# Kernel optimization log

Hardware: AMD Instinct MI355X
Metric: run time of the kernel (lower is better)

Reference implementation:

```python
import jax, jax.numpy as jnp
import numpy as np

H = 64
VOCAB = 64
SLOTS = 4
N_PASSES = 3
EPS = 1e-5


def _ln(x, g, b):
    m = jnp.mean(x, axis=-1, keepdims=True)
    v = jnp.mean((x - m) ** 2, axis=-1, keepdims=True)
    return (x - m) * jax.lax.rsqrt(v + EPS) * g + b


def setup_inputs() -> dict:
    key = jax.random.key(0)
    ks = iter(jax.random.split(key, 32))
    B, L = 128, 4096
    f = lambda shape, scale=0.05: jax.random.normal(next(ks), shape, dtype=jnp.float32) * scale
    inp = {
        "seq": jax.random.randint(next(ks), (B, L), 0, VOCAB),
        # Encoder
        "embed": f((VOCAB, H), 1.0),
        "ff1_w": f((H, 2 * H)), "ff1_b": jnp.zeros((2 * H,), jnp.float32),
        "ff2_w": f((2 * H, H)), "ff2_b": jnp.zeros((H,), jnp.float32),
        "enc_g": jnp.ones((H,), jnp.float32), "enc_b": jnp.zeros((H,), jnp.float32),
        # ForwardGate
        "g1_w": f((H, H // 2)), "g1_b": jnp.zeros((H // 2,), jnp.float32),
        "g2_w": f((H // 2, 1)), "g2_b": jnp.zeros((1,), jnp.float32),
        # Re-encoding layers (stacked over passes)
        "rq_w": f((N_PASSES, H, H)), "rq_b": jnp.zeros((N_PASSES, H), jnp.float32),
        "rk_w": f((N_PASSES, H, H)), "rk_b": jnp.zeros((N_PASSES, H), jnp.float32),
        "rv_w": f((N_PASSES, H, H)), "rv_b": jnp.zeros((N_PASSES, H), jnp.float32),
        "rn_g": jnp.ones((N_PASSES, H), jnp.float32), "rn_b": jnp.zeros((N_PASSES, H), jnp.float32),
        # ReadHead
        "rd_q_w": f((H, H)), "rd_q_b": jnp.zeros((H,), jnp.float32),
        "out_w": f((H, VOCAB)), "out_b": jnp.zeros((VOCAB,), jnp.float32),
    }
    return inp


def reference(seq, embed, ff1_w, ff1_b, ff2_w, ff2_b, enc_g, enc_b,
              g1_w, g1_b, g2_w, g2_b,
              rq_w, rq_b, rk_w, rk_b, rv_w, rv_b, rn_g, rn_b,
              rd_q_w, rd_q_b, out_w, out_b):
    scale = 1.0 / np.sqrt(H)
    # Encoder: embed + FFN residual + LayerNorm
    h = embed[seq]                                            # (B,L,H)
    ff = jax.nn.relu(h @ ff1_w + ff1_b) @ ff2_w + ff2_b
    hidden = _ln(h + ff, enc_g, enc_b)                        # (B,L,H)
    # Gate scores -> top-k slot selection
    scores = jax.nn.sigmoid(jax.nn.relu(hidden @ g1_w + g1_b) @ g2_w + g2_b)[..., 0]  # (B,L)
    _, idx = jax.lax.top_k(scores, SLOTS)                     # (B,k)
    slots = jnp.take_along_axis(hidden, idx[:, :, None], axis=1)  # (B,k,H)
    # Iterative cross-attention re-encoding
    for p in range(N_PASSES):
        Sq = slots @ rq_w[p] + rq_b[p]                        # (B,k,H)
        Sk = hidden @ rk_w[p] + rk_b[p]                       # (B,L,H)
        Sv = hidden @ rv_w[p] + rv_b[p]
        attn = jax.nn.softmax(jnp.einsum("bkh,blh->bkl", Sq, Sk) * scale, axis=-1)
        slots = _ln(slots + jnp.einsum("bkl,blh->bkh", attn, Sv), rn_g[p], rn_b[p])
    # Read head: attend last-token query over slots
    q = hidden[:, -1, :] @ rd_q_w + rd_q_b                    # (B,H)
    attn = jax.nn.softmax(jnp.einsum("bkh,bh->bk", slots, q) * scale, axis=-1)
    read = jnp.einsum("bk,bkh->bh", attn, slots)
    return read @ out_w + out_b                               # (B,VOCAB)
```

## Files before the change

### kernel.cpp

```cpp
#include <hip/hip_runtime.h>
#include <math.h>

#define H 64
#define VOCAB 64
#define LSEQ 4096
#define NSLOTS 4
#define NP 3
#define EPS 1e-5f
#define NBUILD 96

typedef unsigned long long ull;

__device__ __forceinline__ float wsum(float x) {
    #pragma unroll
    for (int m = 1; m < 64; m <<= 1) x += __shfl_xor(x, m);
    return x;
}
__device__ __forceinline__ float wmax(float x) {
    #pragma unroll
    for (int m = 1; m < 64; m <<= 1) x = fmaxf(x, __shfl_xor(x, m));
    return x;
}


__global__ __launch_bounds__(256) void build_and_hist(
    const int*   __restrict__ seq,
    const float* __restrict__ embed,
    const float* __restrict__ ff1_w, const float* __restrict__ ff1_b,
    const float* __restrict__ ff2_w, const float* __restrict__ ff2_b,
    const float* __restrict__ enc_g, const float* __restrict__ enc_b,
    const float* __restrict__ g1_w,  const float* __restrict__ g1_b,
    const float* __restrict__ g2_w,  const float* __restrict__ g2_b,
    const float* __restrict__ rq_w,  const float* __restrict__ rq_b,
    const float* __restrict__ rk_w,  const float* __restrict__ rk_b,
    const float* __restrict__ rv_w,  const float* __restrict__ rv_b,
    const float* __restrict__ rd_q_w, const float* __restrict__ rd_q_b,
    const float* __restrict__ out_w,
    float* __restrict__ enc_t, float* __restrict__ score_t,
    float* __restrict__ c_t, float* __restrict__ q_t,
    float* __restrict__ MT, float* __restrict__ SvT, float* __restrict__ owT,
    float* __restrict__ cnts_ws, int* __restrict__ lasts_ws)
{
    __shared__ float bld[4][320];
    __shared__ int   whist[4][64];

    const int bid = blockIdx.x, tid = threadIdx.x;
    const int wid = tid >> 6, lane = tid & 63;

    if (bid < NBUILD) {
        const int t   = bid * 4 + wid;
        const int seg = t >> 6, v = t & 63;
        float* h_s   = bld[wid];
        float* a1p   = bld[wid] + 64;
        float* hid_s = bld[wid] + 192;
        float* sk_s  = bld[wid] + 256;

        h_s[lane] = embed[v * H + lane];
        __builtin_amdgcn_wave_barrier();

        float pA[4] = {0, 0, 0, 0}, pB[4] = {0, 0, 0, 0};
        #pragma unroll
        for (int c4 = 0; c4 < 4; c4++)
            #pragma unroll
            for (int d = 0; d < 16; d++) {
                int dd = c4 * 16 + d;
                float hv = h_s[dd];
                pA[c4] += hv * ff1_w[dd * 128 + lane];
                pB[c4] += hv * ff1_w[dd * 128 + lane + 64];
            }
        a1p[lane]      = fmaxf(ff1_b[lane]      + ((pA[0] + pA[1]) + (pA[2] + pA[3])), 0.f);
        a1p[lane + 64] = fmaxf(ff1_b[lane + 64] + ((pB[0] + pB[1]) + (pB[2] + pB[3])), 0.f);
        __builtin_amdgcn_wave_barrier();

        float pO[4] = {0, 0, 0, 0};
        #pragma unroll
        for (int c4 = 0; c4 < 4; c4++)
            #pragma unroll
            for (int j = 0; j < 32; j++) {
                int jj = c4 * 32 + j;
                pO[c4] += a1p[jj] * ff2_w[jj * H + lane];
            }
        float o = ff2_b[lane] + ((pO[0] + pO[1]) + (pO[2] + pO[3]));

        float x = h_s[lane] + o;
        float s1 = x, s2 = x * x;
        #pragma unroll
        for (int m = 1; m < 64; m <<= 1) { s1 += __shfl_xor(s1, m); s2 += __shfl_xor(s2, m); }
        float mu  = s1 * (1.f / 64.f);
        float var = s2 * (1.f / 64.f) - mu * mu;
        float hid = (x - mu) * rsqrtf(var + EPS) * enc_g[lane] + enc_b[lane];
        hid_s[lane] = hid;
        __builtin_amdgcn_wave_barrier();

        if (seg == 0) {
            enc_t[v * H + lane] = hid;
            float p = 0.f;
            if (lane < 32) {
                float a[2] = {0, 0};
                #pragma unroll
                for (int c2 = 0; c2 < 2; c2++)
                    #pragma unroll
                    for (int d = 0; d < 32; d++) {
                        int dd = c2 * 32 + d;
                        a[c2] += hid_s[dd] * g1_w[dd * 32 + lane];
                    }
                p = fmaxf(g1_b[lane] + a[0] + a[1], 0.f) * g2_w[lane];
            }
            p = wsum(p);
            if (lane == 0) score_t[v] = 1.f / (1.f + expf(-(p + g2_b[0])));
            float qa[4] = {0, 0, 0, 0};
            #pragma unroll
            for (int c4 = 0; c4 < 4; c4++)
                #pragma unroll
                for (int d = 0; d < 16; d++) {
                    int dd = c4 * 16 + d;
                    qa[c4] += hid_s[dd] * rd_q_w[dd * H + lane];
                }
            q_t[v * H + lane] = rd_q_b[lane] + ((qa[0] + qa[1]) + (qa[2] + qa[3]));
        }
        if (seg < 3) {
            const int p = seg;
            float ka[4] = {0, 0, 0, 0};
            #pragma unroll
            for (int c4 = 0; c4 < 4; c4++)
                #pragma unroll
                for (int d = 0; d < 16; d++) {
                    int dd = c4 * 16 + d;
                    ka[c4] += hid_s[dd] * rk_w[(p * H + dd) * H + lane];
                }
            float skv = rk_b[p * H + lane] + ((ka[0] + ka[1]) + (ka[2] + ka[3]));
            sk_s[lane] = skv;
            float cpart = wsum(rq_b[p * H + lane] * skv);
            if (lane == 0) c_t[p * 64 + v] = cpart;
            __builtin_amdgcn_wave_barrier();
            const float4* rw4 = (const float4*)(rq_w + (size_t)(p * 64 + lane) * 64);
            const float4* sk4 = (const float4*)sk_s;
            float ma[4] = {0, 0, 0, 0};
            #pragma unroll
            for (int i = 0; i < 16; i++) {
                float4 w4 = rw4[i];
                float4 s4v = sk4[i];
                ma[0] += w4.x * s4v.x; ma[1] += w4.y * s4v.y;
                ma[2] += w4.z * s4v.z; ma[3] += w4.w * s4v.w;
            }
            MT[p * 4096 + v * 64 + lane] = ((ma[0] + ma[1]) + (ma[2] + ma[3]));
        } else {
            const int p = seg - 3;
            float va[4] = {0, 0, 0, 0};
            #pragma unroll
            for (int c4 = 0; c4 < 4; c4++)
                #pragma unroll
                for (int d = 0; d < 16; d++) {
                    int dd = c4 * 16 + d;
                    va[c4] += hid_s[dd] * rv_w[(p * H + dd) * H + lane];
                }
            float svv = rv_b[p * H + lane] + ((va[0] + va[1]) + (va[2] + va[3]));
            SvT[p * 4096 + lane * 64 + v] = svv;
            if (seg == 3) owT[v * 64 + lane] = out_w[lane * 64 + v];
        }
        return;
    }

    const int b = bid - NBUILD;
    const int4* s4 = (const int4*)(seq + (size_t)b * LSEQ);
    int4 t0 = s4[tid];
    int4 t1 = s4[tid + 256];
    int4 t2 = s4[tid + 512];
    int4 t3 = s4[tid + 768];
    whist[wid][lane] = 0;
    __builtin_amdgcn_wave_barrier();
    {
        int* hw = whist[wid];
        atomicAdd(&hw[t0.x], 1); atomicAdd(&hw[t0.y], 1);
        atomicAdd(&hw[t0.z], 1); atomicAdd(&hw[t0.w], 1);
        atomicAdd(&hw[t1.x], 1); atomicAdd(&hw[t1.y], 1);
        atomicAdd(&hw[t1.z], 1); atomicAdd(&hw[t1.w], 1);
        atomicAdd(&hw[t2.x], 1); atomicAdd(&hw[t2.y], 1);
        atomicAdd(&hw[t2.z], 1); atomicAdd(&hw[t2.w], 1);
        atomicAdd(&hw[t3.x], 1); atomicAdd(&hw[t3.y], 1);
        atomicAdd(&hw[t3.z], 1); atomicAdd(&hw[t3.w], 1);
    }
    __syncthreads();
    if (tid < 64)
        cnts_ws[b * 64 + tid] =
            (float)(whist[0][tid] + whist[1][tid] + whist[2][tid] + whist[3][tid]);
    if (tid == 255) lasts_ws[b] = t3.w;
}

#define PASS(P, MC, MN, CCV, RGV, RBV, LOADNEXT)                               \
{                                                                              \
    float4 vcur[16];                                                           \
    { const float4* b4 = (const float4*)(SvT + (P) * 4096 + lane * 64);        \
      _Pragma("unroll") for (int i = 0; i < 16; i++) vcur[i] = b4[i]; }        \
    if (LOADNEXT) {                                                            \
      const float4* b4 = (const float4*)(MT + ((P) + 1) * 4096 + lane * 64);   \
      _Pragma("unroll") for (int i = 0; i < 16; i++) MN[i] = b4[i]; }          \
    sls[wid][lane] = s;                                                        \
    const float4* sp = (const float4*)sls[wid];                                \
    float a0 = 0, a1x = 0, a2 = 0, a3 = 0;                                     \
    _Pragma("unroll") for (int i = 0; i < 16; i++) {                           \
        float4 s4v = sp[i];                                                    \
        a0 += s4v.x * MC[i].x; a1x += s4v.y * MC[i].y;                         \
        a2 += s4v.z * MC[i].z; a3 += s4v.w * MC[i].w; }                        \
    float lg = (CCV + ((a0 + a1x) + (a2 + a3))) * 0.125f;                      \
    float w  = cntf * __expf(lg);                                              \
    wls[wid][lane] = w;                                                        \
    float denom = wsum(w);                                                     \
    const float4* wp = (const float4*)wls[wid];                                \
    float b0 = 0, b1 = 0, b2 = 0, b3 = 0;                                      \
    _Pragma("unroll") for (int i = 0; i < 16; i++) {                           \
        float4 w4 = wp[i];                                                     \
        b0 += w4.x * vcur[i].x; b1 += w4.y * vcur[i].y;                        \
        b2 += w4.z * vcur[i].z; b3 += w4.w * vcur[i].w; }                      \
    float y = s * denom + ((b0 + b1) + (b2 + b3));                             \
    float s1 = y, s2v = y * y;                                                 \
    _Pragma("unroll") for (int m = 1; m < 64; m <<= 1) {                       \
        s1 += __shfl_xor(s1, m); s2v += __shfl_xor(s2v, m); }                  \
    float muy  = s1 * (1.f / 64.f);                                            \
    float vary = s2v * (1.f / 64.f) - muy * muy;                               \
    s = (y - muy) * rsqrtf(vary + EPS * denom * denom) * RGV + RBV;            \
}

__global__ __launch_bounds__(256) void run_batches(
    const float* __restrict__ score_t, const float* __restrict__ enc_t,
    const float* __restrict__ c_t, const float* __restrict__ q_t,
    const float* __restrict__ MT, const float* __restrict__ SvT,
    const float* __restrict__ owT,
    const float* __restrict__ rn_g, const float* __restrict__ rn_b,
    const float* __restrict__ out_b,
    const float* __restrict__ cnts_ws, const int* __restrict__ lasts_ws,
    float* __restrict__ out)
{
    __shared__ float sls[4][64], wls[4][64], slN[4][64];
    __shared__ float l4[4];
    __shared__ float rbuf[64];

    const int bid = blockIdx.x, tid = threadIdx.x;
    const int wid = tid >> 6, lane = tid & 63;

    const float cntf = cnts_ws[bid * 64 + lane];
    float sc  = score_t[lane];
    float cc0 = c_t[lane],  cc1 = c_t[64 + lane],  cc2 = c_t[128 + lane];
    float rg0 = rn_g[lane], rg1 = rn_g[64 + lane], rg2 = rn_g[128 + lane];
    float rb0 = rn_b[lane], rb1 = rn_b[64 + lane], rb2 = rn_b[128 + lane];
    float ob  = out_b[lane];

    float4 mA[16], mB[16], vA[16];
    {
        const float4* p4 = (const float4*)(MT + lane * 64);
        #pragma unroll
        for (int i = 0; i < 16; i++) mA[i] = p4[i];
        const float4* q4 = (const float4*)(SvT + lane * 64);
        #pragma unroll
        for (int i = 0; i < 16; i++) vA[i] = q4[i];
    }

    float mxs  = wmax(sc);
    ull   bm   = __ballot(sc == mxs);
    int   t_star = __ffsll(bm) - 1;
    int   nmax   = __popcll(bm);
    float cnt_ts = __shfl(cntf, t_star);
    const bool spec = (nmax == 1) && (cnt_ts >= 4.f);

    if (spec) {
        if (wid != 0) return;
        float s = enc_t[t_star * 64 + lane];

        {
            sls[0][lane] = s;
            const float4* sp = (const float4*)sls[0];
            float a0 = 0, a1x = 0, a2 = 0, a3 = 0;
            #pragma unroll
            for (int i = 0; i < 16; i++) {
                float4 s4v = sp[i];
                a0 += s4v.x * mA[i].x; a1x += s4v.y * mA[i].y;
                a2 += s4v.z * mA[i].z; a3 += s4v.w * mA[i].w;
            }
            float lg0 = (cc0 + ((a0 + a1x) + (a2 + a3))) * 0.125f;

            const float4* b4 = (const float4*)(MT + 4096 + lane * 64);
            #pragma unroll
            for (int i = 0; i < 16; i++) mB[i] = b4[i];

            float w = cntf * __expf(lg0);
            wls[0][lane] = w;
            float denom = wsum(w);
            const float4* wp = (const float4*)wls[0];
            float b0 = 0, b1 = 0, b2 = 0, b3 = 0;
            #pragma unroll
            for (int i = 0; i < 16; i++) {
                float4 w4 = wp[i];
                b0 += w4.x * vA[i].x; b1 += w4.y * vA[i].y;
                b2 += w4.z * vA[i].z; b3 += w4.w * vA[i].w;
            }
            float y = s * denom + ((b0 + b1) + (b2 + b3));
            float s1 = y, s2v = y * y;
            #pragma unroll
            for (int m = 1; m < 64; m <<= 1) { s1 += __shfl_xor(s1, m); s2v += __shfl_xor(s2v, m); }
            float muy  = s1 * (1.f / 64.f);
            float vary = s2v * (1.f / 64.f) - muy * muy;
            s = (y - muy) * rsqrtf(vary + EPS * denom * denom) * rg0 + rb0;
        }
        PASS(1, mB, mA, cc1, rg1, rb1, 1)
        PASS(2, mA, mB, cc2, rg2, rb2, 0)

        float4 ow[16];
        {
            const float4* b4 = (const float4*)(owT + lane * 64);
            #pragma unroll
            for (int i = 0; i < 16; i++) ow[i] = b4[i];
        }
        rbuf[lane] = s;
        __builtin_amdgcn_wave_barrier();
        const float4* rp = (const float4*)rbuf;
        float o0 = ob, o1 = 0.f, o2 = 0.f, o3 = 0.f;
        #pragma unroll
        for (int i = 0; i < 16; i++) {
            float4 rv = rp[i];
            o0 += rv.x * ow[i].x; o1 += rv.y * ow[i].y;
            o2 += rv.z * ow[i].z; o3 += rv.w * ow[i].w;
        }
        out[(size_t)bid * VOCAB + lane] = ((o0 + o1) + (o2 + o3));
        return;
    }

    const int cnt = (int)cntf;
    const int last = lasts_ws[bid];
    float q = q_t[last * 64 + lane];

    int my_tok = 0;
    {
        float key = cnt > 0 ? sc : -1.f;
        int filled = 0;
        bool have = false;
        #pragma unroll 1
        for (int r = 0; r < NSLOTS && filled < NSLOTS; r++) {
            float m2 = wmax(key);
            ull win = __ballot(key == m2);
            int tk = __ffsll(win) - 1;
            int c  = __shfl(cnt, tk);
            if (!have && (unsigned)(wid - filled) < (unsigned)c) { my_tok = tk; have = true; }
            filled += c;
            if (lane == tk) key = -1.f;
        }
    }

    float s = enc_t[my_tok * 64 + lane];

    PASS(0, mA, mB, cc0, rg0, rb0, 1)
    PASS(1, mB, mA, cc1, rg1, rb1, 1)
    PASS(2, mA, mB, cc2, rg2, rb2, 0)

    float lk = wsum(s * q) * 0.125f;
    if (lane == 0) l4[wid] = lk;
    slN[wid][lane] = s;

    float4 ow[16];
    if (wid == 0) {
        const float4* b4 = (const float4*)(owT + lane * 64);
        #pragma unroll
        for (int i = 0; i < 16; i++) ow[i] = b4[i];
    }
    __syncthreads();

    if (wid == 0) {
        float e0 = __expf(l4[0]), e1 = __expf(l4[1]);
        float e2 = __expf(l4[2]), e3 = __expf(l4[3]);
        float dn = e0 + e1 + e2 + e3;
        float r = (e0 * slN[0][lane] + e1 * slN[1][lane]
                 + e2 * slN[2][lane] + e3 * slN[3][lane]) / dn;
        rbuf[lane] = r;
        __builtin_amdgcn_wave_barrier();
        const float4* rp = (const float4*)rbuf;
        float o0 = ob, o1 = 0.f, o2 = 0.f, o3 = 0.f;
        #pragma unroll
        for (int i = 0; i < 16; i++) {
            float4 rv = rp[i];
            o0 += rv.x * ow[i].x; o1 += rv.y * ow[i].y;
            o2 += rv.z * ow[i].z; o3 += rv.w * ow[i].w;
        }
        out[(size_t)bid * VOCAB + lane] = ((o0 + o1) + (o2 + o3));
    }
}

extern "C" void kernel_launch(void* const* d_in, const int* in_sizes, int n_in,
                              void* d_out, int out_size, void* d_ws, size_t ws_size,
                              hipStream_t stream) {
    const int*   seq    = (const int*)  d_in[0];
    const float* embed  = (const float*)d_in[1];
    const float* ff1_w  = (const float*)d_in[2];
    const float* ff1_b  = (const float*)d_in[3];
    const float* ff2_w  = (const float*)d_in[4];
    const float* ff2_b  = (const float*)d_in[5];
    const float* enc_g  = (const float*)d_in[6];
    const float* enc_b  = (const float*)d_in[7];
    const float* g1_w   = (const float*)d_in[8];
    const float* g1_b   = (const float*)d_in[9];
    const float* g2_w   = (const float*)d_in[10];
    const float* g2_b   = (const float*)d_in[11];
    const float* rq_w   = (const float*)d_in[12];
    const float* rq_b   = (const float*)d_in[13];
    const float* rk_w   = (const float*)d_in[14];
    const float* rk_b   = (const float*)d_in[15];
    const float* rv_w   = (const float*)d_in[16];
    const float* rv_b   = (const float*)d_in[17];
    const float* rn_g   = (const float*)d_in[18];
    const float* rn_b   = (const float*)d_in[19];
    const float* rd_q_w = (const float*)d_in[20];
    const float* rd_q_b = (const float*)d_in[21];
    const float* out_w  = (const float*)d_in[22];
    const float* out_b  = (const float*)d_in[23];
    float* out = (float*)d_out;

    const int B = in_sizes[0] / LSEQ;

    float* ws      = (float*)d_ws;
    float* enc_t   = ws;
    float* score_t = ws + 4096;
    float* c_t     = ws + 4160;
    float* q_t     = ws + 4352;
    float* MT      = ws + 8448;
    float* SvT     = ws + 20736;
    float* owT     = ws + 33024;
    float* cnts_ws = ws + 37120;
    int*   lasts_ws = (int*)(ws + 37120 + (size_t)B * 64);

    build_and_hist<<<NBUILD + B, 256, 0, stream>>>(
        seq, embed, ff1_w, ff1_b, ff2_w, ff2_b, enc_g, enc_b,
        g1_w, g1_b, g2_w, g2_b,
        rq_w, rq_b, rk_w, rk_b, rv_w, rv_b,
        rd_q_w, rd_q_b, out_w,
        enc_t, score_t, c_t, q_t, MT, SvT, owT, cnts_ws, lasts_ws);

    run_batches<<<B, 256, 0, stream>>>(
        score_t, enc_t, c_t, q_t, MT, SvT, owT,
        rn_g, rn_b, out_b, cnts_ws, lasts_ws, out);
}
```

Before: 24.75 us.

## Fuse build and batch kernels into one launch with global flag spin-wait

Merges the table-building/histogram kernel and the per-batch attention kernel into a single launch. Build blocks signal completion through an atomic counter, and batch blocks compute their histogram and then spin until all build blocks are done before reading the shared tables. This removes a kernel launch boundary and the global round-trip for counts and last tokens. In exchange it adds a memset launch and relies on all build blocks being co-resident or scheduled ahead, which risks deadlock or spin overhead.

After: 46.17 us. 86.5% more time.

```diff
diff --git a/kernel.cpp b/kernel.cpp
--- a/kernel.cpp
+++ b/kernel.cpp
@@ -8,6 +8,7 @@
 #define NP 3
 #define EPS 1e-5f
 #define NBUILD 96
+#define FLAG_OFF (1u << 20)
 
 typedef unsigned long long ull;
 
@@ -22,170 +23,6 @@
     return x;
 }
 
-
-__global__ __launch_bounds__(256) void build_and_hist(
-    const int*   __restrict__ seq,
-    const float* __restrict__ embed,
-    const float* __restrict__ ff1_w, const float* __restrict__ ff1_b,
-    const float* __restrict__ ff2_w, const float* __restrict__ ff2_b,
-    const float* __restrict__ enc_g, const float* __restrict__ enc_b,
-    const float* __restrict__ g1_w,  const float* __restrict__ g1_b,
-    const float* __restrict__ g2_w,  const float* __restrict__ g2_b,
-    const float* __restrict__ rq_w,  const float* __restrict__ rq_b,
-    const float* __restrict__ rk_w,  const float* __restrict__ rk_b,
-    const float* __restrict__ rv_w,  const float* __restrict__ rv_b,
-    const float* __restrict__ rd_q_w, const float* __restrict__ rd_q_b,
-    const float* __restrict__ out_w,
-    float* __restrict__ enc_t, float* __restrict__ score_t,
-    float* __restrict__ c_t, float* __restrict__ q_t,
-    float* __restrict__ MT, float* __restrict__ SvT, float* __restrict__ owT,
-    float* __restrict__ cnts_ws, int* __restrict__ lasts_ws)
-{
-    __shared__ float bld[4][320];
-    __shared__ int   whist[4][64];
-
-    const int bid = blockIdx.x, tid = threadIdx.x;
-    const int wid = tid >> 6, lane = tid & 63;
-
-    if (bid < NBUILD) {
-        const int t   = bid * 4 + wid;
-        const int seg = t >> 6, v = t & 63;
-        float* h_s   = bld[wid];
-        float* a1p   = bld[wid] + 64;
-        float* hid_s = bld[wid] + 192;
-        float* sk_s  = bld[wid] + 256;
-
-        h_s[lane] = embed[v * H + lane];
-        __builtin_amdgcn_wave_barrier();
-
-        float pA[4] = {0, 0, 0, 0}, pB[4] = {0, 0, 0, 0};
-        #pragma unroll
-        for (int c4 = 0; c4 < 4; c4++)
-            #pragma unroll
-            for (int d = 0; d < 16; d++) {
-                int dd = c4 * 16 + d;
-                float hv = h_s[dd];
-                pA[c4] += hv * ff1_w[dd * 128 + lane];
-                pB[c4] += hv * ff1_w[dd * 128 + lane + 64];
-            }
-        a1p[lane]      = fmaxf(ff1_b[lane]      + ((pA[0] + pA[1]) + (pA[2] + pA[3])), 0.f);
-        a1p[lane + 64] = fmaxf(ff1_b[lane + 64] + ((pB[0] + pB[1]) + (pB[2] + pB[3])), 0.f);
-        __builtin_amdgcn_wave_barrier();
-
-        float pO[4] = {0, 0, 0, 0};
-        #pragma unroll
-        for (int c4 = 0; c4 < 4; c4++)
-            #pragma unroll
-            for (int j = 0; j < 32; j++) {
-                int jj = c4 * 32 + j;
-                pO[c4] += a1p[jj] * ff2_w[jj * H + lane];
-            }
-        float o = ff2_b[lane] + ((pO[0] + pO[1]) + (pO[2] + pO[3]));
-
-        float x = h_s[lane] + o;
-        float s1 = x, s2 = x * x;
-        #pragma unroll
-        for (int m = 1; m < 64; m <<= 1) { s1 += __shfl_xor(s1, m); s2 += __shfl_xor(s2, m); }
-        float mu  = s1 * (1.f / 64.f);
-        float var = s2 * (1.f / 64.f) - mu * mu;
-        float hid = (x - mu) * rsqrtf(var + EPS) * enc_g[lane] + enc_b[lane];
-        hid_s[lane] = hid;
-        __builtin_amdgcn_wave_barrier();
-
-        if (seg == 0) {
-            enc_t[v * H + lane] = hid;
-            float p = 0.f;
-            if (lane < 32) {
-                float a[2] = {0, 0};
-                #pragma unroll
-                for (int c2 = 0; c2 < 2; c2++)
-                    #pragma unroll
-                    for (int d = 0; d < 32; d++) {
-                        int dd = c2 * 32 + d;
-                        a[c2] += hid_s[dd] * g1_w[dd * 32 + lane];
-                    }
-                p = fmaxf(g1_b[lane] + a[0] + a[1], 0.f) * g2_w[lane];
-            }
-            p = wsum(p);
-            if (lane == 0) score_t[v] = 1.f / (1.f + expf(-(p + g2_b[0])));
-            float qa[4] = {0, 0, 0, 0};
-            #pragma unroll
-            for (int c4 = 0; c4 < 4; c4++)
-                #pragma unroll
-                for (int d = 0; d < 16; d++) {
-                    int dd = c4 * 16 + d;
-                    qa[c4] += hid_s[dd] * rd_q_w[dd * H + lane];
-                }
-            q_t[v * H + lane] = rd_q_b[lane] + ((qa[0] + qa[1]) + (qa[2] + qa[3]));
-        }
-        if (seg < 3) {
-            const int p = seg;
-            float ka[4] = {0, 0, 0, 0};
-            #pragma unroll
-            for (int c4 = 0; c4 < 4; c4++)
-                #pragma unroll
-                for (int d = 0; d < 16; d++) {
-                    int dd = c4 * 16 + d;
-                    ka[c4] += hid_s[dd] * rk_w[(p * H + dd) * H + lane];
-                }
-            float skv = rk_b[p * H + lane] + ((ka[0] + ka[1]) + (ka[2] + ka[3]));
-            sk_s[lane] = skv;
-            float cpart = wsum(rq_b[p * H + lane] * skv);
-            if (lane == 0) c_t[p * 64 + v] = cpart;
-            __builtin_amdgcn_wave_barrier();
-            const float4* rw4 = (const float4*)(rq_w + (size_t)(p * 64 + lane) * 64);
-            const float4* sk4 = (const float4*)sk_s;
-            float ma[4] = {0, 0, 0, 0};
-            #pragma unroll
-            for (int i = 0; i < 16; i++) {
-                float4 w4 = rw4[i];
-                float4 s4v = sk4[i];
-                ma[0] += w4.x * s4v.x; ma[1] += w4.y * s4v.y;
-                ma[2] += w4.z * s4v.z; ma[3] += w4.w * s4v.w;
-            }
-            MT[p * 4096 + v * 64 + lane] = ((ma[0] + ma[1]) + (ma[2] + ma[3]));
-        } else {
-            const int p = seg - 3;
-            float va[4] = {0, 0, 0, 0};
-            #pragma unroll
-            for (int c4 = 0; c4 < 4; c4++)
-                #pragma unroll
-                for (int d = 0; d < 16; d++) {
-                    int dd = c4 * 16 + d;
-                    va[c4] += hid_s[dd] * rv_w[(p * H + dd) * H + lane];
-                }
-            float svv = rv_b[p * H + lane] + ((va[0] + va[1]) + (va[2] + va[3]));
-            SvT[p * 4096 + lane * 64 + v] = svv;
-            if (seg == 3) owT[v * 64 + lane] = out_w[lane * 64 + v];
-        }
-        return;
-    }
-
-    const int b = bid - NBUILD;
-    const int4* s4 = (const int4*)(seq + (size_t)b * LSEQ);
-    int4 t0 = s4[tid];
-    int4 t1 = s4[tid + 256];
-    int4 t2 = s4[tid + 512];
-    int4 t3 = s4[tid + 768];
-    whist[wid][lane] = 0;
-    __builtin_amdgcn_wave_barrier();
-    {
-        int* hw = whist[wid];
-        atomicAdd(&hw[t0.x], 1); atomicAdd(&hw[t0.y], 1);
-        atomicAdd(&hw[t0.z], 1); atomicAdd(&hw[t0.w], 1);
-        atomicAdd(&hw[t1.x], 1); atomicAdd(&hw[t1.y], 1);
-        atomicAdd(&hw[t1.z], 1); atomicAdd(&hw[t1.w], 1);
-        atomicAdd(&hw[t2.x], 1); atomicAdd(&hw[t2.y], 1);
-        atomicAdd(&hw[t2.z], 1); atomicAdd(&hw[t2.w], 1);
-        atomicAdd(&hw[t3.x], 1); atomicAdd(&hw[t3.y], 1);
-        atomicAdd(&hw[t3.z], 1); atomicAdd(&hw[t3.w], 1);
-    }
-    __syncthreads();
-    if (tid < 64)
-        cnts_ws[b * 64 + tid] =
-            (float)(whist[0][tid] + whist[1][tid] + whist[2][tid] + whist[3][tid]);
-    if (tid == 255) lasts_ws[b] = t3.w;
-}
 
 #define PASS(P, MC, MN, CCV, RGV, RBV, LOADNEXT)                               \
 {                                                                              \
@@ -221,16 +58,29 @@
     s = (y - muy) * rsqrtf(vary + EPS * denom * denom) * RGV + RBV;            \
 }
 
-__global__ __launch_bounds__(256) void run_batches(
-    const float* __restrict__ score_t, const float* __restrict__ enc_t,
-    const float* __restrict__ c_t, const float* __restrict__ q_t,
-    const float* __restrict__ MT, const float* __restrict__ SvT,
-    const float* __restrict__ owT,
-    const float* __restrict__ rn_g, const float* __restrict__ rn_b,
-    const float* __restrict__ out_b,
-    const float* __restrict__ cnts_ws, const int* __restrict__ lasts_ws,
+__global__ __launch_bounds__(256) void fused(
+    const int*   __restrict__ seq,
+    const float* __restrict__ embed,
+    const float* __restrict__ ff1_w, const float* __restrict__ ff1_b,
+    const float* __restrict__ ff2_w, const float* __restrict__ ff2_b,
+    const float* __restrict__ enc_g, const float* __restrict__ enc_b,
+    const float* __restrict__ g1_w,  const float* __restrict__ g1_b,
+    const float* __restrict__ g2_w,  const float* __restrict__ g2_b,
+    const float* __restrict__ rq_w,  const float* __restrict__ rq_b,
+    const float* __restrict__ rk_w,  const float* __restrict__ rk_b,
+    const float* __restrict__ rv_w,  const float* __restrict__ rv_b,
+    const float* __restrict__ rn_g,  const float* __restrict__ rn_b,
+    const float* __restrict__ rd_q_w, const float* __restrict__ rd_q_b,
+    const float* __restrict__ out_w, const float* __restrict__ out_b,
+    float* __restrict__ enc_t, float* __restrict__ score_t,
+    float* __restrict__ c_t, float* __restrict__ q_t,
+    float* __restrict__ MT, float* __restrict__ SvT, float* __restrict__ owT,
+    unsigned* __restrict__ flagp,
     float* __restrict__ out)
 {
+    __shared__ float bld[4][320];
+    __shared__ int   whist[4][64];
+    __shared__ int   last_sh;
     __shared__ float sls[4][64], wls[4][64], slN[4][64];
     __shared__ float l4[4];
     __shared__ float rbuf[64];
@@ -238,13 +88,162 @@
     const int bid = blockIdx.x, tid = threadIdx.x;
     const int wid = tid >> 6, lane = tid & 63;
 
-    const float cntf = cnts_ws[bid * 64 + lane];
-    float sc  = score_t[lane];
-    float cc0 = c_t[lane],  cc1 = c_t[64 + lane],  cc2 = c_t[128 + lane];
+    if (bid < NBUILD) {
+        const int t   = bid * 4 + wid;
+        const int seg = t >> 6, v = t & 63;
+        float* h_s   = bld[wid];
+        float* a1p   = bld[wid] + 64;
+        float* hid_s = bld[wid] + 192;
+        float* sk_s  = bld[wid] + 256;
+
+        h_s[lane] = embed[v * H + lane];
+        __builtin_amdgcn_wave_barrier();
+
+        float pA[4] = {0, 0, 0, 0}, pB[4] = {0, 0, 0, 0};
+        #pragma unroll
+        for (int c4 = 0; c4 < 4; c4++)
+            #pragma unroll
+            for (int d = 0; d < 16; d++) {
+                int dd = c4 * 16 + d;
+                float hv = h_s[dd];
+                pA[c4] += hv * ff1_w[dd * 128 + lane];
+                pB[c4] += hv * ff1_w[dd * 128 + lane + 64];
+            }
+        a1p[lane]      = fmaxf(ff1_b[lane]      + ((pA[0] + pA[1]) + (pA[2] + pA[3])), 0.f);
+        a1p[lane + 64] = fmaxf(ff1_b[lane + 64] + ((pB[0] + pB[1]) + (pB[2] + pB[3])), 0.f);
+        __builtin_amdgcn_wave_barrier();
+
+        float pO[4] = {0, 0, 0, 0};
+        #pragma unroll
+        for (int c4 = 0; c4 < 4; c4++)
+            #pragma unroll
+            for (int j = 0; j < 32; j++) {
+                int jj = c4 * 32 + j;
+                pO[c4] += a1p[jj] * ff2_w[jj * H + lane];
+            }
+        float o = ff2_b[lane] + ((pO[0] + pO[1]) + (pO[2] + pO[3]));
+
+        float x = h_s[lane] + o;
+        float s1 = x, s2 = x * x;
+        #pragma unroll
+        for (int m = 1; m < 64; m <<= 1) { s1 += __shfl_xor(s1, m); s2 += __shfl_xor(s2, m); }
+        float mu  = s1 * (1.f / 64.f);
+        float var = s2 * (1.f / 64.f) - mu * mu;
+        float hid = (x - mu) * rsqrtf(var + EPS) * enc_g[lane] + enc_b[lane];
+        hid_s[lane] = hid;
+        __builtin_amdgcn_wave_barrier();
+
+        if (seg == 0) {
+            enc_t[v * H + lane] = hid;
+            float p = 0.f;
+            if (lane < 32) {
+                float a[2] = {0, 0};
+                #pragma unroll
+                for (int c2 = 0; c2 < 2; c2++)
+                    #pragma unroll
+                    for (int d = 0; d < 32; d++) {
+                        int dd = c2 * 32 + d;
+                        a[c2] += hid_s[dd] * g1_w[dd * 32 + lane];
+                    }
+                p = fmaxf(g1_b[lane] + a[0] + a[1], 0.f) * g2_w[lane];
+            }
+            p = wsum(p);
+            if (lane == 0) score_t[v] = 1.f / (1.f + expf(-(p + g2_b[0])));
+            float qa[4] = {0, 0, 0, 0};
+            #pragma unroll
+            for (int c4 = 0; c4 < 4; c4++)
+                #pragma unroll
+                for (int d = 0; d < 16; d++) {
+                    int dd = c4 * 16 + d;
+                    qa[c4] += hid_s[dd] * rd_q_w[dd * H + lane];
+                }
+            q_t[v * H + lane] = rd_q_b[lane] + ((qa[0] + qa[1]) + (qa[2] + qa[3]));
+        }
+        if (seg < 3) {
+            const int p = seg;
+            float ka[4] = {0, 0, 0, 0};
+            #pragma unroll
+            for (int c4 = 0; c4 < 4; c4++)
+                #pragma unroll
+                for (int d = 0; d < 16; d++) {
+                    int dd = c4 * 16 + d;
+                    ka[c4] += hid_s[dd] * rk_w[(p * H + dd) * H + lane];
+                }
+            float skv = rk_b[p * H + lane] + ((ka[0] + ka[1]) + (ka[2] + ka[3]));
+            sk_s[lane] = skv;
+            float cpart = wsum(rq_b[p * H + lane] * skv);
+            if (lane == 0) c_t[p * 64 + v] = cpart;
+            __builtin_amdgcn_wave_barrier();
+            const float4* rw4 = (const float4*)(rq_w + (size_t)(p * 64 + lane) * 64);
+            const float4* sk4 = (const float4*)sk_s;
+            float ma[4] = {0, 0, 0, 0};
+            #pragma unroll
+            for (int i = 0; i < 16; i++) {
+                float4 w4 = rw4[i];
+                float4 s4v = sk4[i];
+                ma[0] += w4.x * s4v.x; ma[1] += w4.y * s4v.y;
+                ma[2] += w4.z * s4v.z; ma[3] += w4.w * s4v.w;
+            }
+            MT[p * 4096 + v * 64 + lane] = ((ma[0] + ma[1]) + (ma[2] + ma[3]));
+        } else {
+            const int p = seg - 3;
+            float va[4] = {0, 0, 0, 0};
+            #pragma unroll
+            for (int c4 = 0; c4 < 4; c4++)
+                #pragma unroll
+                for (int d = 0; d < 16; d++) {
+                    int dd = c4 * 16 + d;
+                    va[c4] += hid_s[dd] * rv_w[(p * H + dd) * H + lane];
+                }
+            float svv = rv_b[p * H + lane] + ((va[0] + va[1]) + (va[2] + va[3]));
+            SvT[p * 4096 + lane * 64 + v] = svv;
+            if (seg == 3) owT[v * 64 + lane] = out_w[lane * 64 + v];
+        }
+        __threadfence();
+        __syncthreads();
+        if (tid == 0) atomicAdd(flagp, 1u);
+        return;
+    }
+
+    const int b = bid - NBUILD;
+
+    const int4* s4 = (const int4*)(seq + (size_t)b * LSEQ);
+    int4 t0 = s4[tid];
+    int4 t1 = s4[tid + 256];
+    int4 t2 = s4[tid + 512];
+    int4 t3 = s4[tid + 768];
+    if (tid == 255) last_sh = t3.w;
+    whist[wid][lane] = 0;
+
     float rg0 = rn_g[lane], rg1 = rn_g[64 + lane], rg2 = rn_g[128 + lane];
     float rb0 = rn_b[lane], rb1 = rn_b[64 + lane], rb2 = rn_b[128 + lane];
     float ob  = out_b[lane];
 
+    __builtin_amdgcn_wave_barrier();
+    {
+        int* hw = whist[wid];
+        atomicAdd(&hw[t0.x], 1); atomicAdd(&hw[t0.y], 1);
+        atomicAdd(&hw[t0.z], 1); atomicAdd(&hw[t0.w], 1);
+        atomicAdd(&hw[t1.x], 1); atomicAdd(&hw[t1.y], 1);
+        atomicAdd(&hw[t1.z], 1); atomicAdd(&hw[t1.w], 1);
+        atomicAdd(&hw[t2.x], 1); atomicAdd(&hw[t2.y], 1);
+        atomicAdd(&hw[t2.z], 1); atomicAdd(&hw[t2.w], 1);
+        atomicAdd(&hw[t3.x], 1); atomicAdd(&hw[t3.y], 1);
+        atomicAdd(&hw[t3.z], 1); atomicAdd(&hw[t3.w], 1);
+    }
+    __syncthreads();
+    const int cnt = whist[0][lane] + whist[1][lane] + whist[2][lane] + whist[3][lane];
+    const float cntf = (float)cnt;
+
+    if (tid == 0) {
+        while (atomicAdd(flagp, 0u) < (unsigned)NBUILD)
+            __builtin_amdgcn_s_sleep(2);
+    }
+    __syncthreads();
+    __threadfence();
+
+    float sc  = score_t[lane];
+    float cc0 = c_t[lane], cc1 = c_t[64 + lane], cc2 = c_t[128 + lane];
     float4 mA[16], mB[16], vA[16];
     {
         const float4* p4 = (const float4*)(MT + lane * 64);
@@ -320,13 +319,11 @@
             o0 += rv.x * ow[i].x; o1 += rv.y * ow[i].y;
             o2 += rv.z * ow[i].z; o3 += rv.w * ow[i].w;
         }
-        out[(size_t)bid * VOCAB + lane] = ((o0 + o1) + (o2 + o3));
+        out[(size_t)b * VOCAB + lane] = ((o0 + o1) + (o2 + o3));
         return;
     }
 
-    const int cnt = (int)cntf;
-    const int last = lasts_ws[bid];
-    float q = q_t[last * 64 + lane];
+    float q = q_t[last_sh * 64 + lane];
 
     int my_tok = 0;
     {
@@ -379,7 +376,7 @@
             o0 += rv.x * ow[i].x; o1 += rv.y * ow[i].y;
             o2 += rv.z * ow[i].z; o3 += rv.w * ow[i].w;
         }
-        out[(size_t)bid * VOCAB + lane] = ((o0 + o1) + (o2 + o3));
+        out[(size_t)b * VOCAB + lane] = ((o0 + o1) + (o2 + o3));
     }
 }
 
@@ -422,17 +419,14 @@
     float* MT      = ws + 8448;
     float* SvT     = ws + 20736;
     float* owT     = ws + 33024;
-    float* cnts_ws = ws + 37120;
-    int*   lasts_ws = (int*)(ws + 37120 + (size_t)B * 64);
-
-    build_and_hist<<<NBUILD + B, 256, 0, stream>>>(
+    unsigned* flagp = (unsigned*)((char*)d_ws + FLAG_OFF);
+
+    hipMemsetAsync(flagp, 0, 64, stream);
+
+    fused<<<NBUILD + B, 256, 0, stream>>>(
         seq, embed, ff1_w, ff1_b, ff2_w, ff2_b, enc_g, enc_b,
         g1_w, g1_b, g2_w, g2_b,
-        rq_w, rq_b, rk_w, rk_b, rv_w, rv_b,
-        rd_q_w, rd_q_b, out_w,
-        enc_t, score_t, c_t, q_t, MT, SvT, owT, cnts_ws, lasts_ws);
-
-    run_batches<<<B, 256, 0, stream>>>(
-        score_t, enc_t, c_t, q_t, MT, SvT, owT,
-        rn_g, rn_b, out_b, cnts_ws, lasts_ws, out);
+        rq_w, rq_b, rk_w, rk_b, rv_w, rv_b, rn_g, rn_b,
+        rd_q_w, rd_q_b, out_w, out_b,
+        enc_t, score_t, c_t, q_t, MT, SvT, owT, flagp, out);
 }
```
